# Kernel optimization log

Hardware: AMD Instinct MI355X
Metric: run time of the kernel (lower is better)

The kernel has to match this reference:

```python
import jax, jax.numpy as jnp
import numpy as np

NTYPES = 2
MAXNEI = 128      # maxNeighborNum
M2 = 16
NPER = 256        # atoms per type
B = 4
EMB = [25, 50, 100]
FIT_IN = M2 * EMB[-1]  # 1600
FH = 240


def setup_inputs() -> dict:
    key = jax.random.key(0)
    ks = jax.random.split(key, 16)
    s = 0.1
    inp = {
        "Ri": jax.random.normal(ks[0], (B, NTYPES * NPER, NTYPES * MAXNEI, 4), jnp.float32),
        "emb_W0": jax.random.normal(ks[1], (4, 1, EMB[0]), jnp.float32) * s,
        "emb_b0": jax.random.normal(ks[2], (4, EMB[0]), jnp.float32) * s,
        "emb_W1": jax.random.normal(ks[3], (4, EMB[0], EMB[1]), jnp.float32) * s,
        "emb_b1": jax.random.normal(ks[4], (4, EMB[1]), jnp.float32) * s,
        "emb_W2": jax.random.normal(ks[5], (4, EMB[1], EMB[2]), jnp.float32) * s,
        "emb_b2": jax.random.normal(ks[6], (4, EMB[2]), jnp.float32) * s,
        "fit_W0": jax.random.normal(ks[7], (2, FIT_IN, FH), jnp.float32) * 0.02,
        "fit_b0": jax.random.normal(ks[8], (2, FH), jnp.float32) * s,
        "fit_W1": jax.random.normal(ks[9], (2, FH, FH), jnp.float32) * 0.05,
        "fit_b1": jax.random.normal(ks[10], (2, FH), jnp.float32) * s,
        "fit_W2": jax.random.normal(ks[11], (2, FH, FH), jnp.float32) * 0.05,
        "fit_b2": jax.random.normal(ks[12], (2, FH), jnp.float32) * s,
        "fit_W3": jax.random.normal(ks[13], (2, FH, 1), jnp.float32) * 0.05,
        "fit_b3": jax.random.normal(ks[14], (2, 1), jnp.float32),
    }
    return inp


def _emb(s, W0, b0, W1, b1, W2, b2):
    # DeepMD-style embedding MLP with doubling resnet skips (1->25->50->100)
    h0 = jnp.tanh(s @ W0 + b0)
    h1 = jnp.tanh(h0 @ W1 + b1) + jnp.concatenate([h0, h0], axis=-1)
    h2 = jnp.tanh(h1 @ W2 + b2) + jnp.concatenate([h1, h1], axis=-1)
    return h2


def _fit(d, W0, b0, W1, b1, W2, b2, W3, b3):
    h = jnp.tanh(d @ W0 + b0)
    h = jnp.tanh(h @ W1 + b1) + h   # resnet skip (equal dims)
    h = jnp.tanh(h @ W2 + b2) + h
    return h @ W3 + b3              # [B, N, 1]


def reference(Ri, emb_W0, emb_b0, emb_W1, emb_b1, emb_W2, emb_b2,
              fit_W0, fit_b0, fit_W1, fit_b1, fit_W2, fit_b2, fit_W3, fit_b3):
    type_nums = NTYPES
    Ei_blocks = []
    for i in range(NTYPES):                      # center-atom type
        Ri_i = Ri[:, i * NPER:(i + 1) * NPER]    # [B, NPER, NTYPES*M, 4]
        xyz = None
        for j in range(NTYPES):                  # neighbor type
            blk = Ri_i[:, :, j * MAXNEI:(j + 1) * MAXNEI, :]  # [B,N,M,4]
            S = blk[..., 0:1]                                  # [B,N,M,1]
            e = i * NTYPES + j
            G = _emb(S, emb_W0[e], emb_b0[e], emb_W1[e], emb_b1[e],
                     emb_W2[e], emb_b2[e])                     # [B,N,M,100]
            tmp = jnp.einsum('bnmc,bnmg->bncg', blk, G)        # [B,N,4,100]
            xyz = tmp if xyz is None else xyz + tmp
        xyz = xyz / (MAXNEI * type_nums)
        xyz_b = xyz[..., :M2]                                  # [B,N,4,16]
        DR = jnp.einsum('bncg,bnch->bngh', xyz, xyz_b)         # [B,N,100,16]
        DR = DR.reshape(B, NPER, FIT_IN)
        Ei_i = _fit(DR, fit_W0[i], fit_b0[i], fit_W1[i], fit_b1[i],
                    fit_W2[i], fit_b2[i], fit_W3[i], fit_b3[i])  # [B,N,1]
        Ei_blocks.append(Ei_i)
    Ei = jnp.concatenate(Ei_blocks, axis=1)     # [B, natoms_sum, 1]
    return Ei[..., 0]                            # per-atom energies [B, natoms_sum]
```

## Files before the change

kernel.cpp:

```cpp
#include <hip/hip_runtime.h>
#include <hip/hip_bf16.h>

#define FH 240
#define FIT_IN 1600
#define NK 2048
#define TLO -16.0f
#define TINVH 64.0f
#define KSPLIT0 8
#define CHUNK0 200

typedef _Float16 h8 __attribute__((ext_vector_type(8)));
typedef float f4v __attribute__((ext_vector_type(4)));

__device__ __forceinline__ float fast_tanh(float x) {
    float e2 = __builtin_amdgcn_exp2f(x * 2.8853900817779268f);
    return 1.0f - 2.0f * __builtin_amdgcn_rcpf(e2 + 1.0f);
}

#define FMA_ROW(r, s) \
    acc[r][0] += (s) * b0.x; acc[r][1] += (s) * b0.y; \
    acc[r][2] += (s) * b0.z; acc[r][3] += (s) * b0.w; \
    acc[r][4] += (s) * b1.x; acc[r][5] += (s) * b1.y; \
    acc[r][6] += (s) * b1.z; acc[r][7] += (s) * b1.w;

#define TOFF_W0   0
#define TOFF_B0   28
#define TOFF_B1   56
#define TOFF_B2   108
#define TOFF_W1   208
#define TOFF_W2   1508
#define TOFF_H0T  6708
#define TOFF_H1T  10008
#define TSMEM     16608

__global__ __launch_bounds__(256) void k_table(
    const float* __restrict__ eW0, const float* __restrict__ eB0,
    const float* __restrict__ eW1, const float* __restrict__ eB1,
    const float* __restrict__ eW2, const float* __restrict__ eB2,
    float* __restrict__ T)
{
    __shared__ float sm[TSMEM];

    const int t    = threadIdx.x;
    const int w    = t >> 6;
    const int lane = t & 63;
    const int mi   = lane & 7;
    const int gi   = lane >> 3;
    const int mrow = w * 32 + mi * 4;

    const int e  = blockIdx.y;
    const int k0 = blockIdx.x * 128;

    for (int idx = t; idx < 1250; idx += 256) {
        int k = idx / 50, g = idx - k * 50;
        sm[TOFF_W1 + k * 52 + g] = eW1[e * 1250 + idx];
    }
    for (int idx = t; idx < 5000; idx += 256) {
        int k = idx / 100, r = idx - k * 100;
        int half = r / 50, g = r - half * 50;
        sm[TOFF_W2 + k * 104 + half * 52 + g] = eW2[e * 5000 + idx];
    }
    if (t < 25)       { sm[TOFF_W0 + t] = eW0[e * 25 + t]; sm[TOFF_B0 + t] = eB0[e * 25 + t]; }
    else if (t < 75)  { sm[TOFF_B1 + (t - 25)] = eB1[e * 50 + (t - 25)]; }
    else if (t < 175) { sm[TOFF_B2 + (t - 75)] = eB2[e * 100 + (t - 75)]; }
    __syncthreads();

    if (t < 128) {
        const float S = TLO + (float)(k0 + t) * (1.0f / TINVH);
        #pragma unroll
        for (int k = 0; k < 25; ++k)
            sm[TOFF_H0T + k * 132 + t] = fast_tanh(S * sm[TOFF_W0 + k] + sm[TOFF_B0 + k]);
    }
    __syncthreads();

    {
        float acc[4][8];
        #pragma unroll
        for (int r = 0; r < 4; ++r)
            #pragma unroll
            for (int c = 0; c < 8; ++c) acc[r][c] = 0.f;

        #pragma unroll 5
        for (int k = 0; k < 25; ++k) {
            const float4 av = *(const float4*)&sm[TOFF_H0T + k * 132 + mrow];
            const float4 b0 = *(const float4*)&sm[TOFF_W1 + k * 52 + gi * 8];
            const float4 b1 = *(const float4*)&sm[TOFF_W1 + k * 52 + gi * 8 + 4];
            FMA_ROW(0, av.x) FMA_ROW(1, av.y) FMA_ROW(2, av.z) FMA_ROW(3, av.w)
        }
        #pragma unroll
        for (int c = 0; c < 8; ++c) {
            const int g = gi * 8 + c;
            if (g < 50) {
                const int gm = (g < 25) ? g : g - 25;
                const float4 h0r = *(const float4*)&sm[TOFF_H0T + gm * 132 + mrow];
                const float bias = sm[TOFF_B1 + g];
                float4 o;
                o.x = fast_tanh(acc[0][c] + bias) + h0r.x;
                o.y = fast_tanh(acc[1][c] + bias) + h0r.y;
                o.z = fast_tanh(acc[2][c] + bias) + h0r.z;
                o.w = fast_tanh(acc[3][c] + bias) + h0r.w;
                *(float4*)&sm[TOFF_H1T + g * 132 + mrow] = o;
            }
        }
    }
    __syncthreads();

    for (int half = 0; half < 2; ++half) {
        float acc[4][8];
        #pragma unroll
        for (int r = 0; r < 4; ++r)
            #pragma unroll
            for (int c = 0; c < 8; ++c) acc[r][c] = 0.f;

        #pragma unroll 5
        for (int k = 0; k < 50; ++k) {
            const float4 av = *(const float4*)&sm[TOFF_H1T + k * 132 + mrow];
            const float4 b0 = *(const float4*)&sm[TOFF_W2 + k * 104 + half * 52 + gi * 8];
            const float4 b1 = *(const float4*)&sm[TOFF_W2 + k * 104 + half * 52 + gi * 8 + 4];
            FMA_ROW(0, av.x) FMA_ROW(1, av.y) FMA_ROW(2, av.z) FMA_ROW(3, av.w)
        }
        #pragma unroll
        for (int c = 0; c < 8; ++c) {
            const int g = gi * 8 + c;
            if (g < 50) {
                const float4 h1r = *(const float4*)&sm[TOFF_H1T + g * 132 + mrow];
                const float bias = sm[TOFF_B2 + half * 50 + g];
                float* out = T + ((size_t)e * NK + k0 + mrow) * 100 + half * 50 + g;
                out[0]   = fast_tanh(acc[0][c] + bias) + h1r.x;
                out[100] = fast_tanh(acc[1][c] + bias) + h1r.y;
                out[200] = fast_tanh(acc[2][c] + bias) + h1r.z;
                out[300] = fast_tanh(acc[3][c] + bias) + h1r.w;
            }
        }
    }
}

__global__ __launch_bounds__(256) void k_cvt(
    const float* __restrict__ fW0, const float* __restrict__ fW1,
    const float* __restrict__ fW2,
    _Float16* __restrict__ W0T, _Float16* __restrict__ W1T,
    _Float16* __restrict__ W2T)
{
    const int total = 768000 + 115200 + 115200;
    for (int idx = blockIdx.x * 256 + threadIdx.x; idx < total; idx += gridDim.x * 256) {
        if (idx < 768000) {
            const int tp = idx / 384000, r = idx - tp * 384000;
            const int n = r / 1600, k = r - n * 1600;
            W0T[idx] = (_Float16)fW0[tp * 384000 + k * 240 + n];
        } else if (idx < 883200) {
            const int j = idx - 768000;
            const int tp = j / 57600, r = j - tp * 57600;
            const int n = r / 240, k = r - n * 240;
            W1T[j] = (_Float16)fW1[tp * 57600 + k * 240 + n];
        } else {
            const int j = idx - 883200;
            const int tp = j / 57600, r = j - tp * 57600;
            const int n = r / 240, k = r - n * 240;
            W2T[j] = (_Float16)fW2[tp * 57600 + k * 240 + n];
        }
    }
}

__global__ __launch_bounds__(256) void k_xyz(
    const float* __restrict__ Ri, const float* __restrict__ T,
    _Float16* __restrict__ DRh)
{
    __shared__ float4 sR[256];
    __shared__ float  sF[256];
    __shared__ int    sI[256];
    __shared__ float  sXYZ[400];

    const int t   = threadIdx.x;
    const int blk = blockIdx.x;
    const int b   = blk >> 9;
    const int i   = (blk >> 8) & 1;
    const int n   = blk & 255;

    for (int idx = t; idx < 400; idx += 256) sXYZ[idx] = 0.f;

    {
        const int jj = t >> 7, m = t & 127;
        const size_t row = ((size_t)(b * 512 + i * 256 + n)) * 256 + jj * 128 + m;
        const float4 r = *(const float4*)(Ri + row * 4);
        sR[t] = r;
        float u = (r.x - TLO) * TINVH;
        int ii = (int)u;
        ii = (ii < 0) ? 0 : ((ii > NK - 2) ? NK - 2 : ii);
        sI[t] = ii;
        sF[t] = u - (float)ii;
    }
    __syncthreads();

    const int jj = t >> 7;
    const int g  = t & 127;
    if (g < 100) {
        const float* Te = T + ((size_t)(i * 2 + jj)) * NK * 100 + g;
        float a0 = 0.f, a1 = 0.f, a2 = 0.f, a3 = 0.f;
        #pragma unroll 4
        for (int m = 0; m < 128; ++m) {
            const int s = jj * 128 + m;
            const float4 R = sR[s];
            const float  f = sF[s];
            const float* p = Te + (size_t)sI[s] * 100;
            const float v0 = p[0], v1 = p[100];
            const float G = v0 + f * (v1 - v0);
            a0 += R.x * G; a1 += R.y * G; a2 += R.z * G; a3 += R.w * G;
        }
        atomicAdd(&sXYZ[g],       a0);
        atomicAdd(&sXYZ[100 + g], a1);
        atomicAdd(&sXYZ[200 + g], a2);
        atomicAdd(&sXYZ[300 + g], a3);
    }
    __syncthreads();

    const float inv = 1.0f / 65536.0f;
    _Float16* dr = DRh + (((size_t)i * 4 + b) * 256 + n) * FIT_IN;
    for (int q = t; q < 400; q += 256) {
        const int gg = q >> 2, h0 = (q & 3) * 4;
        ushort4 pk;
        _Float16* ph = (_Float16*)&pk;
        #pragma unroll
        for (int r = 0; r < 4; ++r) {
            const int h = h0 + r;
            const float v = (sXYZ[gg] * sXYZ[h] + sXYZ[100 + gg] * sXYZ[100 + h]
                           + sXYZ[200 + gg] * sXYZ[200 + h] + sXYZ[300 + gg] * sXYZ[300 + h]) * inv;
            ph[r] = (_Float16)v;
        }
        *(ushort4*)(dr + gg * 16 + h0) = pk;
    }
}

template<int K, int CHUNK>
__global__ __launch_bounds__(256) void k_fit_mfma(
    const _Float16* __restrict__ A, const _Float16* __restrict__ WT,
    float* __restrict__ P)
{
    __shared__ _Float16 sA[32 * 40];
    __shared__ _Float16 sBT[240 * 40];

    const int t    = threadIdx.x;
    const int w    = t >> 6;
    const int lane = t & 63;
    const int ln   = lane & 15;
    const int quad = lane >> 4;

    const int mtile = blockIdx.x;
    const int ks    = blockIdx.y;
    const int row0  = mtile * 32;
    const int tp    = mtile >> 5;
    const int kbeg  = ks * CHUNK;
    const int kend  = (kbeg + CHUNK < K) ? (kbeg + CHUNK) : K;
    const int nf0   = w * 4;
    const int nfrags = (w < 3) ? 4 : 3;

    f4v acc[2][4];
    #pragma unroll
    for (int mf = 0; mf < 2; ++mf)
        #pragma unroll
        for (int nf = 0; nf < 4; ++nf) acc[mf][nf] = (f4v)0.f;

    const _Float16* Ab = A + (size_t)row0 * K;
    const _Float16* Wb = WT + (size_t)tp * 240 * K;

    for (int k0 = kbeg; k0 < kend; k0 += 32) {
        {
            const int m = t >> 3, kq = (t & 7) * 4;
            const int k = k0 + kq;
            uint2 v = make_uint2(0u, 0u);
            if (k < kend) v = *(const uint2*)(Ab + (size_t)m * K + k);
            *(uint2*)&sA[m * 40 + kq] = v;
        }
        for (int q = t; q < 1920; q += 256) {
            const int n = q >> 3, kq = (q & 7) * 4;
            const int k = k0 + kq;
            uint2 v = make_uint2(0u, 0u);
            if (k < kend) v = *(const uint2*)(Wb + (size_t)n * K + k);
            *(uint2*)&sBT[n * 40 + kq] = v;
        }
        __syncthreads();

        h8 afr[2];
        #pragma unroll
        for (int mf = 0; mf < 2; ++mf)
            afr[mf] = *(const h8*)&sA[(mf * 16 + ln) * 40 + quad * 8];
        #pragma unroll
        for (int nf = 0; nf < 4; ++nf) {
            if (nf < nfrags) {
                const h8 bfr = *(const h8*)&sBT[((nf0 + nf) * 16 + ln) * 40 + quad * 8];
                #pragma unroll
                for (int mf = 0; mf < 2; ++mf)
                    acc[mf][nf] = __builtin_amdgcn_mfma_f32_16x16x32_f16(
                        afr[mf], bfr, acc[mf][nf], 0, 0, 0);
            }
        }
        __syncthreads();
    }

    float* Pb = P + ((size_t)ks * 2048 + row0) * FH;
    #pragma unroll
    for (int nf = 0; nf < 4; ++nf) {
        if (nf < nfrags) {
            const int col = (nf0 + nf) * 16 + ln;
            #pragma unroll
            for (int mf = 0; mf < 2; ++mf)
                #pragma unroll
                for (int r = 0; r < 4; ++r) {
                    const int row = mf * 16 + quad * 4 + r;
                    Pb[(size_t)row * FH + col] = acc[mf][nf][r];
                }
        }
    }
}

__global__ __launch_bounds__(256) void k_fit_tail(
    const float* __restrict__ P,
    const _Float16* __restrict__ W1T, const _Float16* __restrict__ W2T,
    const float* __restrict__ fb0, const float* __restrict__ fb1,
    const float* __restrict__ fb2, const float* __restrict__ fW3,
    const float* __restrict__ fb3, float* __restrict__ out)
{
    __shared__ float    hRes[2][16 * 240];
    __shared__ _Float16 sA[16 * 264];
    __shared__ _Float16 sB[240 * 40];

    const int t    = threadIdx.x;
    const int w    = t >> 6;
    const int lane = t & 63;
    const int ln   = lane & 15;
    const int quad = lane >> 4;
    const int r0   = blockIdx.x * 16;
    const int tp   = r0 >> 10;
    const int nf0  = w * 4;
    const int nfrags = (w < 3) ? 4 : 3;

    #pragma unroll
    for (int j = 0; j < 15; ++j) {
        const int e = t + j * 256;
        const int m = e / 240, col = e - m * 240;
        const size_t base = (size_t)(r0 + m) * FH + col;
        float s = 0.f;
        #pragma unroll
        for (int ks = 0; ks < KSPLIT0; ++ks)
            s += P[(size_t)ks * 2048 * FH + base];
        const float v = fast_tanh(s + fb0[tp * FH + col]);
        hRes[0][m * 240 + col] = v;
        sA[m * 264 + col] = (_Float16)v;
    }
    if (t < 256) {
        const int m = t >> 4, c = 240 + (t & 15);
        sA[m * 264 + c] = (_Float16)0.f;
    }

    #pragma unroll
    for (int layer = 0; layer < 2; ++layer) {
        const _Float16* Wt = (layer == 0 ? W1T : W2T) + (size_t)tp * FH * FH;
        const float* Bias  = (layer == 0 ? fb1 : fb2) + tp * FH;
        const float* res   = hRes[layer];
        float* outb        = hRes[layer ^ 1];

        f4v acc[4];
        #pragma unroll
        for (int nf = 0; nf < 4; ++nf) acc[nf] = (f4v)0.f;

        for (int k0 = 0; k0 < 256; k0 += 32) {
            __syncthreads();
            for (int q = t; q < 1920; q += 256) {
                const int n = q >> 3, kq = (q & 7) * 4;
                const int k = k0 + kq;
                uint2 v = make_uint2(0u, 0u);
                if (k < FH) v = *(const uint2*)(Wt + (size_t)n * FH + k);
                *(uint2*)&sB[n * 40 + kq] = v;
            }
            __syncthreads();
            const h8 afr = *(const h8*)&sA[ln * 264 + k0 + quad * 8];
            #pragma unroll
            for (int nf = 0; nf < 4; ++nf) {
                if (nf < nfrags) {
                    const h8 bfr = *(const h8*)&sB[((nf0 + nf) * 16 + ln) * 40 + quad * 8];
                    acc[nf] = __builtin_amdgcn_mfma_f32_16x16x32_f16(afr, bfr, acc[nf], 0, 0, 0);
                }
            }
        }
        __syncthreads();

        #pragma unroll
        for (int nf = 0; nf < 4; ++nf) {
            if (nf < nfrags) {
                const int col = (nf0 + nf) * 16 + ln;
                const float bias = Bias[col];
                #pragma unroll
                for (int r = 0; r < 4; ++r) {
                    const int m = quad * 4 + r;
                    const float v = fast_tanh(acc[nf][r] + bias) + res[m * 240 + col];
                    outb[m * 240 + col] = v;
                    if (layer == 0) sA[m * 264 + col] = (_Float16)v;
                }
            }
        }
        __syncthreads();
    }

    const float* h2 = hRes[0];
    const float* wv = fW3 + tp * FH;
    #pragma unroll
    for (int rr = 0; rr < 4; ++rr) {
        const int m = w * 4 + rr;
        float s = 0.f;
        for (int k = lane; k < FH; k += 64)
            s += h2[m * 240 + k] * wv[k];
        #pragma unroll
        for (int off = 32; off > 0; off >>= 1) s += __shfl_down(s, off);
        if (lane == 0) {
            const int gr = r0 + m;
            const int b = (gr >> 8) & 3, n = gr & 255;
            out[b * 512 + tp * 256 + n] = s + fb3[tp];
        }
    }
}

extern "C" void kernel_launch(void* const* d_in, const int* in_sizes, int n_in,
                              void* d_out, int out_size, void* d_ws, size_t ws_size,
                              hipStream_t stream)
{
    const float* Ri  = (const float*)d_in[0];
    const float* eW0 = (const float*)d_in[1];
    const float* eB0 = (const float*)d_in[2];
    const float* eW1 = (const float*)d_in[3];
    const float* eB1 = (const float*)d_in[4];
    const float* eW2 = (const float*)d_in[5];
    const float* eB2 = (const float*)d_in[6];
    const float* fW0 = (const float*)d_in[7];
    const float* fb0 = (const float*)d_in[8];
    const float* fW1 = (const float*)d_in[9];
    const float* fb1 = (const float*)d_in[10];
    const float* fW2 = (const float*)d_in[11];
    const float* fb2 = (const float*)d_in[12];
    const float* fW3 = (const float*)d_in[13];
    const float* fb3 = (const float*)d_in[14];

    char* p = (char*)d_ws;
    float* T   = (float*)p;                 p += (size_t)4 * NK * 100 * 4;
    float* P   = (float*)p;                 p += (size_t)KSPLIT0 * 2048 * FH * 4;
    _Float16* DRh = (_Float16*)p;           p += (size_t)2048 * FIT_IN * 2;
    _Float16* W0T = (_Float16*)p;           p += (size_t)768000 * 2;
    _Float16* W1T = (_Float16*)p;           p += (size_t)115200 * 2;
    _Float16* W2T = (_Float16*)p;           p += (size_t)115200 * 2;

    k_cvt<<<dim3(1024), dim3(256), 0, stream>>>(fW0, fW1, fW2, W0T, W1T, W2T);
    k_table<<<dim3(NK / 128, 4), dim3(256), 0, stream>>>(eW0, eB0, eW1, eB1, eW2, eB2, T);
    k_xyz<<<dim3(2048), dim3(256), 0, stream>>>(Ri, T, DRh);

    k_fit_mfma<FIT_IN, CHUNK0><<<dim3(64, KSPLIT0), dim3(256), 0, stream>>>(DRh, W0T, P);

    k_fit_tail<<<dim3(128), dim3(256), 0, stream>>>(P, W1T, W2T, fb0, fb1, fb2, fW3, fb3,
                                                    (float*)d_out);
}
```

Measured before the change: 196.7 us.

## Fuse split-K fitting layer into tail kernel and merge prep kernels

Merges the weight conversion and embedding table kernels into one launch by partitioning the block index. Replaces the split-K first fitting layer, which wrote partial sums to a workspace, and the separate tail kernel with one fused 512-thread kernel. Each block now runs all fitting layers for 8 rows, with register-prefetched, double-buffered weight tiles. This removes two launches and the partial-sum round trip through global memory. In exchange each block streams the whole 1600x240 layer-0 weight for only 8 rows (half the MFMA tile is padding), so weight traffic rises and K-parallelism falls.

```diff
diff --git a/kernel.cpp b/kernel.cpp
--- a/kernel.cpp
+++ b/kernel.cpp
@@ -6,8 +6,6 @@
 #define NK 2048
 #define TLO -16.0f
 #define TINVH 64.0f
-#define KSPLIT0 8
-#define CHUNK0 200
 
 typedef _Float16 h8 __attribute__((ext_vector_type(8)));
 typedef float f4v __attribute__((ext_vector_type(4)));
@@ -33,23 +31,50 @@
 #define TOFF_H1T  10008
 #define TSMEM     16608
 
-__global__ __launch_bounds__(256) void k_table(
+__global__ __launch_bounds__(256) void k_prep(
     const float* __restrict__ eW0, const float* __restrict__ eB0,
     const float* __restrict__ eW1, const float* __restrict__ eB1,
     const float* __restrict__ eW2, const float* __restrict__ eB2,
-    float* __restrict__ T)
+    float* __restrict__ T,
+    const float* __restrict__ fW0, const float* __restrict__ fW1,
+    const float* __restrict__ fW2,
+    _Float16* __restrict__ W0T, _Float16* __restrict__ W1T,
+    _Float16* __restrict__ W2T)
 {
     __shared__ float sm[TSMEM];
-
-    const int t    = threadIdx.x;
+    const int t = threadIdx.x;
+
+    if (blockIdx.x >= 64) {
+        const int bid0 = blockIdx.x - 64;
+        const int total = 768000 + 115200 + 115200;
+        for (int idx = bid0 * 256 + t; idx < total; idx += 448 * 256) {
+            if (idx < 768000) {
+                const int tp = idx / 384000, r = idx - tp * 384000;
+                const int n = r / 1600, k = r - n * 1600;
+                W0T[idx] = (_Float16)fW0[tp * 384000 + k * 240 + n];
+            } else if (idx < 883200) {
+                const int j = idx - 768000;
+                const int tp = j / 57600, r = j - tp * 57600;
+                const int n = r / 240, k = r - n * 240;
+                W1T[j] = (_Float16)fW1[tp * 57600 + k * 240 + n];
+            } else {
+                const int j = idx - 883200;
+                const int tp = j / 57600, r = j - tp * 57600;
+                const int n = r / 240, k = r - n * 240;
+                W2T[j] = (_Float16)fW2[tp * 57600 + k * 240 + n];
+            }
+        }
+        return;
+    }
+
     const int w    = t >> 6;
     const int lane = t & 63;
     const int mi   = lane & 7;
     const int gi   = lane >> 3;
     const int mrow = w * 32 + mi * 4;
 
-    const int e  = blockIdx.y;
-    const int k0 = blockIdx.x * 128;
+    const int e  = blockIdx.x >> 4;
+    const int k0 = (blockIdx.x & 15) * 128;
 
     for (int idx = t; idx < 1250; idx += 256) {
         int k = idx / 50, g = idx - k * 50;
@@ -131,32 +156,6 @@
                 out[200] = fast_tanh(acc[2][c] + bias) + h1r.z;
                 out[300] = fast_tanh(acc[3][c] + bias) + h1r.w;
             }
-        }
-    }
-}
-
-__global__ __launch_bounds__(256) void k_cvt(
-    const float* __restrict__ fW0, const float* __restrict__ fW1,
-    const float* __restrict__ fW2,
-    _Float16* __restrict__ W0T, _Float16* __restrict__ W1T,
-    _Float16* __restrict__ W2T)
-{
-    const int total = 768000 + 115200 + 115200;
-    for (int idx = blockIdx.x * 256 + threadIdx.x; idx < total; idx += gridDim.x * 256) {
-        if (idx < 768000) {
-            const int tp = idx / 384000, r = idx - tp * 384000;
-            const int n = r / 1600, k = r - n * 1600;
-            W0T[idx] = (_Float16)fW0[tp * 384000 + k * 240 + n];
-        } else if (idx < 883200) {
-            const int j = idx - 768000;
-            const int tp = j / 57600, r = j - tp * 57600;
-            const int n = r / 240, k = r - n * 240;
-            W1T[j] = (_Float16)fW1[tp * 57600 + k * 240 + n];
-        } else {
-            const int j = idx - 883200;
-            const int tp = j / 57600, r = j - tp * 57600;
-            const int n = r / 240, k = r - n * 240;
-            W2T[j] = (_Float16)fW2[tp * 57600 + k * 240 + n];
         }
     }
 }
@@ -230,168 +229,176 @@
     }
 }
 
-template<int K, int CHUNK>
-__global__ __launch_bounds__(256) void k_fit_mfma(
-    const _Float16* __restrict__ A, const _Float16* __restrict__ WT,
-    float* __restrict__ P)
+__global__ __launch_bounds__(512) void k_fit(
+    const _Float16* __restrict__ DRh,
+    const _Float16* __restrict__ W0T, const _Float16* __restrict__ W1T,
+    const _Float16* __restrict__ W2T,
+    const float* __restrict__ fb0, const float* __restrict__ fb1,
+    const float* __restrict__ fb2, const float* __restrict__ fW3,
+    const float* __restrict__ fb3, float* __restrict__ out)
 {
-    __shared__ _Float16 sA[32 * 40];
-    __shared__ _Float16 sBT[240 * 40];
+    __shared__ _Float16 sB[2][240 * 40];
+    __shared__ _Float16 sA0[2][16 * 40];
+    __shared__ _Float16 sA[16 * 264];
+    __shared__ float    hRes[2][8 * 240];
 
     const int t    = threadIdx.x;
     const int w    = t >> 6;
     const int lane = t & 63;
     const int ln   = lane & 15;
     const int quad = lane >> 4;
-
-    const int mtile = blockIdx.x;
-    const int ks    = blockIdx.y;
-    const int row0  = mtile * 32;
-    const int tp    = mtile >> 5;
-    const int kbeg  = ks * CHUNK;
-    const int kend  = (kbeg + CHUNK < K) ? (kbeg + CHUNK) : K;
-    const int nf0   = w * 4;
-    const int nfrags = (w < 3) ? 4 : 3;
-
-    f4v acc[2][4];
-    #pragma unroll
-    for (int mf = 0; mf < 2; ++mf)
-        #pragma unroll
-        for (int nf = 0; nf < 4; ++nf) acc[mf][nf] = (f4v)0.f;
-
-    const _Float16* Ab = A + (size_t)row0 * K;
-    const _Float16* Wb = WT + (size_t)tp * 240 * K;
-
-    for (int k0 = kbeg; k0 < kend; k0 += 32) {
+    const int r0   = blockIdx.x * 8;
+    const int tp   = r0 >> 10;
+    const int nf0  = w * 2;
+    const int nfr  = (w < 7) ? 2 : 1;
+
+    for (int q = t; q < 16 * 264; q += 512) sA[q] = (_Float16)0.f;
+    for (int q = t; q < 2 * 16 * 40; q += 512) ((_Float16*)sA0)[q] = (_Float16)0.f;
+
+    const _Float16* Ab = DRh + (size_t)r0 * FIT_IN;
+    const _Float16* Wb = W0T + (size_t)tp * 240 * FIT_IN;
+
+    f4v acc[2];
+    acc[0] = (f4v)0.f; acc[1] = (f4v)0.f;
+    {
+        uint2 pB[4]; uint2 pA;
         {
-            const int m = t >> 3, kq = (t & 7) * 4;
-            const int k = k0 + kq;
-            uint2 v = make_uint2(0u, 0u);
-            if (k < kend) v = *(const uint2*)(Ab + (size_t)m * K + k);
-            *(uint2*)&sA[m * 40 + kq] = v;
-        }
-        for (int q = t; q < 1920; q += 256) {
-            const int n = q >> 3, kq = (q & 7) * 4;
-            const int k = k0 + kq;
-            uint2 v = make_uint2(0u, 0u);
-            if (k < kend) v = *(const uint2*)(Wb + (size_t)n * K + k);
-            *(uint2*)&sBT[n * 40 + kq] = v;
-        }
-        __syncthreads();
-
-        h8 afr[2];
-        #pragma unroll
-        for (int mf = 0; mf < 2; ++mf)
-            afr[mf] = *(const h8*)&sA[(mf * 16 + ln) * 40 + quad * 8];
-        #pragma unroll
-        for (int nf = 0; nf < 4; ++nf) {
-            if (nf < nfrags) {
-                const h8 bfr = *(const h8*)&sBT[((nf0 + nf) * 16 + ln) * 40 + quad * 8];
+            const int k0 = 0;
+            #pragma unroll
+            for (int j = 0; j < 4; ++j) {
+                const int q = t + j * 512;
+                if (q < 1920) {
+                    const int n = q >> 3, kq = (q & 7) * 4;
+                    pB[j] = *(const uint2*)(Wb + (size_t)n * FIT_IN + k0 + kq);
+                }
+            }
+            if (t < 64) {
+                const int m = t >> 3, kq = (t & 7) * 4;
+                pA = *(const uint2*)(Ab + (size_t)m * FIT_IN + k0 + kq);
+            }
+        }
+        for (int step = 0; step < 50; ++step) {
+            const int buf = step & 1;
+            #pragma unroll
+            for (int j = 0; j < 4; ++j) {
+                const int q = t + j * 512;
+                if (q < 1920) {
+                    const int n = q >> 3, kq = (q & 7) * 4;
+                    *(uint2*)&sB[buf][n * 40 + kq] = pB[j];
+                }
+            }
+            if (t < 64) {
+                const int m = t >> 3, kq = (t & 7) * 4;
+                *(uint2*)&sA0[buf][m * 40 + kq] = pA;
+            }
+            __syncthreads();
+            if (step < 49) {
+                const int k0 = (step + 1) * 32;
                 #pragma unroll
-                for (int mf = 0; mf < 2; ++mf)
-                    acc[mf][nf] = __builtin_amdgcn_mfma_f32_16x16x32_f16(
-                        afr[mf], bfr, acc[mf][nf], 0, 0, 0);
-            }
-        }
-        __syncthreads();
-    }
-
-    float* Pb = P + ((size_t)ks * 2048 + row0) * FH;
-    #pragma unroll
-    for (int nf = 0; nf < 4; ++nf) {
-        if (nf < nfrags) {
-            const int col = (nf0 + nf) * 16 + ln;
-            #pragma unroll
-            for (int mf = 0; mf < 2; ++mf)
+                for (int j = 0; j < 4; ++j) {
+                    const int q = t + j * 512;
+                    if (q < 1920) {
+                        const int n = q >> 3, kq = (q & 7) * 4;
+                        pB[j] = *(const uint2*)(Wb + (size_t)n * FIT_IN + k0 + kq);
+                    }
+                }
+                if (t < 64) {
+                    const int m = t >> 3, kq = (t & 7) * 4;
+                    pA = *(const uint2*)(Ab + (size_t)m * FIT_IN + k0 + kq);
+                }
+            }
+            const h8 afr = *(const h8*)&sA0[buf][ln * 40 + quad * 8];
+            #pragma unroll
+            for (int nf = 0; nf < 2; ++nf) {
+                if (nf < nfr) {
+                    const h8 bfr = *(const h8*)&sB[buf][((nf0 + nf) * 16 + ln) * 40 + quad * 8];
+                    acc[nf] = __builtin_amdgcn_mfma_f32_16x16x32_f16(afr, bfr, acc[nf], 0, 0, 0);
+                }
+            }
+        }
+    }
+    __syncthreads();
+    {
+        const float* B0 = fb0 + tp * FH;
+        #pragma unroll
+        for (int nf = 0; nf < 2; ++nf) {
+            if (nf < nfr && quad < 2) {
+                const int col = (nf0 + nf) * 16 + ln;
+                const float bias = B0[col];
                 #pragma unroll
                 for (int r = 0; r < 4; ++r) {
-                    const int row = mf * 16 + quad * 4 + r;
-                    Pb[(size_t)row * FH + col] = acc[mf][nf][r];
-                }
-        }
-    }
-}
-
-__global__ __launch_bounds__(256) void k_fit_tail(
-    const float* __restrict__ P,
-    const _Float16* __restrict__ W1T, const _Float16* __restrict__ W2T,
-    const float* __restrict__ fb0, const float* __restrict__ fb1,
-    const float* __restrict__ fb2, const float* __restrict__ fW3,
-    const float* __restrict__ fb3, float* __restrict__ out)
-{
-    __shared__ float    hRes[2][16 * 240];
-    __shared__ _Float16 sA[16 * 264];
-    __shared__ _Float16 sB[240 * 40];
-
-    const int t    = threadIdx.x;
-    const int w    = t >> 6;
-    const int lane = t & 63;
-    const int ln   = lane & 15;
-    const int quad = lane >> 4;
-    const int r0   = blockIdx.x * 16;
-    const int tp   = r0 >> 10;
-    const int nf0  = w * 4;
-    const int nfrags = (w < 3) ? 4 : 3;
-
-    #pragma unroll
-    for (int j = 0; j < 15; ++j) {
-        const int e = t + j * 256;
-        const int m = e / 240, col = e - m * 240;
-        const size_t base = (size_t)(r0 + m) * FH + col;
-        float s = 0.f;
-        #pragma unroll
-        for (int ks = 0; ks < KSPLIT0; ++ks)
-            s += P[(size_t)ks * 2048 * FH + base];
-        const float v = fast_tanh(s + fb0[tp * FH + col]);
-        hRes[0][m * 240 + col] = v;
-        sA[m * 264 + col] = (_Float16)v;
-    }
-    if (t < 256) {
-        const int m = t >> 4, c = 240 + (t & 15);
-        sA[m * 264 + c] = (_Float16)0.f;
-    }
-
-    #pragma unroll
+                    const int m = quad * 4 + r;
+                    const float v = fast_tanh(acc[nf][r] + bias);
+                    hRes[0][m * 240 + col] = v;
+                    sA[m * 264 + col] = (_Float16)v;
+                }
+            }
+        }
+    }
+    __syncthreads();
+
     for (int layer = 0; layer < 2; ++layer) {
         const _Float16* Wt = (layer == 0 ? W1T : W2T) + (size_t)tp * FH * FH;
         const float* Bias  = (layer == 0 ? fb1 : fb2) + tp * FH;
         const float* res   = hRes[layer];
         float* outb        = hRes[layer ^ 1];
 
-        f4v acc[4];
-        #pragma unroll
-        for (int nf = 0; nf < 4; ++nf) acc[nf] = (f4v)0.f;
-
-        for (int k0 = 0; k0 < 256; k0 += 32) {
+        f4v a2[2];
+        a2[0] = (f4v)0.f; a2[1] = (f4v)0.f;
+        uint2 pW[4];
+        #pragma unroll
+        for (int j = 0; j < 4; ++j) {
+            const int q = t + j * 512;
+            if (q < 1920) {
+                const int n = q >> 3, kq = (q & 7) * 4;
+                pW[j] = (kq < FH) ? *(const uint2*)(Wt + (size_t)n * FH + kq)
+                                  : make_uint2(0u, 0u);
+            }
+        }
+        for (int step = 0; step < 8; ++step) {
+            const int buf = step & 1;
+            #pragma unroll
+            for (int j = 0; j < 4; ++j) {
+                const int q = t + j * 512;
+                if (q < 1920) {
+                    const int n = q >> 3, kq = (q & 7) * 4;
+                    *(uint2*)&sB[buf][n * 40 + kq] = pW[j];
+                }
+            }
             __syncthreads();
-            for (int q = t; q < 1920; q += 256) {
-                const int n = q >> 3, kq = (q & 7) * 4;
-                const int k = k0 + kq;
-                uint2 v = make_uint2(0u, 0u);
-                if (k < FH) v = *(const uint2*)(Wt + (size_t)n * FH + k);
-                *(uint2*)&sB[n * 40 + kq] = v;
-            }
-            __syncthreads();
+            if (step < 7) {
+                const int k0 = (step + 1) * 32;
+                #pragma unroll
+                for (int j = 0; j < 4; ++j) {
+                    const int q = t + j * 512;
+                    if (q < 1920) {
+                        const int n = q >> 3, kq = (q & 7) * 4;
+                        const int k = k0 + kq;
+                        pW[j] = (k < FH) ? *(const uint2*)(Wt + (size_t)n * FH + k)
+                                         : make_uint2(0u, 0u);
+                    }
+                }
+            }
+            const int k0 = step * 32;
             const h8 afr = *(const h8*)&sA[ln * 264 + k0 + quad * 8];
             #pragma unroll
-            for (int nf = 0; nf < 4; ++nf) {
-                if (nf < nfrags) {
-                    const h8 bfr = *(const h8*)&sB[((nf0 + nf) * 16 + ln) * 40 + quad * 8];
-                    acc[nf] = __builtin_amdgcn_mfma_f32_16x16x32_f16(afr, bfr, acc[nf], 0, 0, 0);
+            for (int nf = 0; nf < 2; ++nf) {
+                if (nf < nfr) {
+                    const h8 bfr = *(const h8*)&sB[buf][((nf0 + nf) * 16 + ln) * 40 + quad * 8];
+                    a2[nf] = __builtin_amdgcn_mfma_f32_16x16x32_f16(afr, bfr, a2[nf], 0, 0, 0);
                 }
             }
         }
         __syncthreads();
-
-        #pragma unroll
-        for (int nf = 0; nf < 4; ++nf) {
-            if (nf < nfrags) {
+        #pragma unroll
+        for (int nf = 0; nf < 2; ++nf) {
+            if (nf < nfr && quad < 2) {
                 const int col = (nf0 + nf) * 16 + ln;
                 const float bias = Bias[col];
                 #pragma unroll
                 for (int r = 0; r < 4; ++r) {
                     const int m = quad * 4 + r;
-                    const float v = fast_tanh(acc[nf][r] + bias) + res[m * 240 + col];
+                    const float v = fast_tanh(a2[nf][r] + bias) + res[m * 240 + col];
                     outb[m * 240 + col] = v;
                     if (layer == 0) sA[m * 264 + col] = (_Float16)v;
                 }
@@ -400,19 +407,19 @@
         __syncthreads();
     }
 
-    const float* h2 = hRes[0];
-    const float* wv = fW3 + tp * FH;
-    #pragma unroll
-    for (int rr = 0; rr < 4; ++rr) {
-        const int m = w * 4 + rr;
+    {
+        const float* h2 = hRes[0];
+        const float* wv = fW3 + tp * FH;
+        const int m = w;
         float s = 0.f;
-        for (int k = lane; k < FH; k += 64)
-            s += h2[m * 240 + k] * wv[k];
+        #pragma unroll
+        for (int k = lane; k < FH; k += 64) s += h2[m * 240 + k] * wv[k];
         #pragma unroll
         for (int off = 32; off > 0; off >>= 1) s += __shfl_down(s, off);
         if (lane == 0) {
             const int gr = r0 + m;
-            const int b = (gr >> 8) & 3, n = gr & 255;
+            const int rem = gr & 1023;
+            const int b = rem >> 8, n = rem & 255;
             out[b * 512 + tp * 256 + n] = s + fb3[tp];
         }
     }
@@ -440,18 +447,15 @@
 
     char* p = (char*)d_ws;
     float* T   = (float*)p;                 p += (size_t)4 * NK * 100 * 4;
-    float* P   = (float*)p;                 p += (size_t)KSPLIT0 * 2048 * FH * 4;
     _Float16* DRh = (_Float16*)p;           p += (size_t)2048 * FIT_IN * 2;
     _Float16* W0T = (_Float16*)p;           p += (size_t)768000 * 2;
     _Float16* W1T = (_Float16*)p;           p += (size_t)115200 * 2;
     _Float16* W2T = (_Float16*)p;           p += (size_t)115200 * 2;
 
-    k_cvt<<<dim3(1024), dim3(256), 0, stream>>>(fW0, fW1, fW2, W0T, W1T, W2T);
-    k_table<<<dim3(NK / 128, 4), dim3(256), 0, stream>>>(eW0, eB0, eW1, eB1, eW2, eB2, T);
+    k_prep<<<dim3(512), dim3(256), 0, stream>>>(eW0, eB0, eW1, eB1, eW2, eB2, T,
+                                                fW0, fW1, fW2, W0T, W1T, W2T);
     k_xyz<<<dim3(2048), dim3(256), 0, stream>>>(Ri, T, DRh);
-
-    k_fit_mfma<FIT_IN, CHUNK0><<<dim3(64, KSPLIT0), dim3(256), 0, stream>>>(DRh, W0T, P);
-
-    k_fit_tail<<<dim3(128), dim3(256), 0, stream>>>(P, W1T, W2T, fb0, fb1, fb2, fW3, fb3,
-                                                    (float*)d_out);
+    k_fit<<<dim3(256), dim3(512), 0, stream>>>(DRh, W0T, W1T, W2T,
+                                               fb0, fb1, fb2, fW3, fb3,
+                                               (float*)d_out);
 }
```

New measurement: 174.2 us. 1.13x faster.
